# Performance work log

Hardware: AMD Instinct MI355X
Metric: run time of the kernel (lower is better)

The kernel has to match this reference:

```python
import jax, jax.numpy as jnp
import numpy as np
from jax import lax

T = 16384
L = 1024  # num_labels; START = L-2, STOP = L-1
NEG = -10000.0


def setup_inputs() -> dict:
    key = jax.random.key(0)
    k1, k2, k3 = jax.random.split(key, 3)
    pred_logits = jax.random.normal(k1, (T, L), dtype=jnp.float32)
    # gold tags avoid the reserved START (L-2) and STOP (L-1) tags
    ref = jax.random.randint(k2, (T,), 0, L - 2)
    transitions = jax.random.normal(k3, (L, L), dtype=jnp.float32)
    transitions = transitions.at[L - 2, :].set(NEG).at[L - 1, :].set(NEG)
    return {"pred_logits": pred_logits, "ref": ref, "transitions": transitions}


def reference(pred_logits, ref, transitions):
    num_labels = transitions.shape[0]
    START = num_labels - 2
    STOP = num_labels - 1

    # ---- forward algorithm (log-sum-exp recurrence over tags) ----
    init = jnp.full((num_labels,), NEG, dtype=pred_logits.dtype).at[START].set(0.0)

    def step(alpha, feat):
        # new_alpha[j] = logsumexp_i(alpha[i] + transitions[j, i]) + feat[j]
        new_alpha = jax.nn.logsumexp(alpha[None, :] + transitions, axis=1) + feat
        return new_alpha, None

    alpha, _ = lax.scan(step, init, pred_logits)
    forward_score = jax.nn.logsumexp(alpha + transitions[STOP])

    # ---- gold path score ----
    prev = jnp.concatenate([jnp.array([START], dtype=ref.dtype), ref[:-1]])
    trans_score = transitions[ref, prev].sum()
    emit_score = jnp.take_along_axis(pred_logits, ref[:, None], axis=1).sum()
    gold_score = trans_score + emit_score + transitions[STOP, ref[-1]]

    # torch returns shape (1,)
    return (forward_score - gold_score).reshape(1)
```

## Files before the change

### kernel.cpp

```cpp
#include <hip/hip_runtime.h>


#define TT    16384
#define LLAB  1024
#define NEGV  -10000.0
#define BQ    32
#define NCH   512
#define KCH   32
#define NPTY  8
#define AGT   __HIP_MEMORY_SCOPE_AGENT

typedef unsigned long long u64;
typedef unsigned int u32;
typedef unsigned short u16;
typedef _Float16 f16;
typedef _Float16 h2 __attribute__((ext_vector_type(2)));
typedef _Float16 f16x8 __attribute__((ext_vector_type(8)));
typedef float f32x4 __attribute__((ext_vector_type(4)));

__device__ __forceinline__ void pub64(u64* p, u64 v) {
  __hip_atomic_store(p, v, __ATOMIC_RELAXED, AGT);
}
__device__ __forceinline__ uint4 ld16_sc(const u32* p) {
  uint4 r;
  asm volatile("global_load_dwordx4 %0, %1, off sc0 sc1"
               : "=v"(r) : "v"(p) : "memory");
  return r;
}
__device__ __forceinline__ u32 pack2(float a, float b) {
  h2 h = {(f16)a, (f16)b};
  return __builtin_bit_cast(u32, h);
}
__device__ __forceinline__ float f16lo(u32 b) {
  return (float)__builtin_bit_cast(f16, (u16)(b & 0xFFFFu));
}
__device__ __forceinline__ float f16hi(u32 b) {
  return (float)__builtin_bit_cast(f16, (u16)(b >> 16));
}
__device__ __forceinline__ int swz(int c, int w) { return w ^ ((c & 7) << 2); }

__device__ __forceinline__ float max8(uint4 v) {
  float m = fmaxf(fmaxf(f16lo(v.x), f16hi(v.x)), fmaxf(f16lo(v.y), f16hi(v.y)));
  m = fmaxf(m, fmaxf(f16lo(v.z), f16hi(v.z)));
  m = fmaxf(m, fmaxf(f16lo(v.w), f16hi(v.w)));
  return m;
}

__global__ __launch_bounds__(256, 1) void crf_chunks(
    const float* __restrict__ pred, const float* __restrict__ trans,
    const int* __restrict__ ref, u32* __restrict__ pay, u32* __restrict__ fl,
    float* __restrict__ ybuf, float* __restrict__ zbuf,
    double* __restrict__ tlog, float* __restrict__ gold) {
  const int tid = threadIdx.x;
  const int wv = tid >> 6, l = tid & 63;
  const int lm = l & 15, lg = l >> 4;
  const int b = blockIdx.x;
  const int g = b & 31;
  const int party = b >> 5;
  const bool isFwd = (g < 16);
  const int cbase = (g & 15) * KCH;
  const int c1 = cbase + lm, c2 = cbase + lm + 16;
  const int tb1 = c1 * BQ, tb2 = c2 * BQ;
  const int wb = 128 * party + 32 * wv;

  f16x8 afrag0[32], afrag1[32];
  if (isFwd) {
    const float4* rp0 = (const float4*)&trans[(size_t)(wb + lm) * LLAB];
    const float4* rp1 = (const float4*)&trans[(size_t)(wb + 16 + lm) * LLAB];
#pragma unroll
    for (int kt = 0; kt < 32; ++kt) {
      float4 a = rp0[8 * kt + 2 * lg], c = rp0[8 * kt + 2 * lg + 1];
      f16x8 f;
      f[0] = (f16)__expf(a.x); f[1] = (f16)__expf(a.y);
      f[2] = (f16)__expf(a.z); f[3] = (f16)__expf(a.w);
      f[4] = (f16)__expf(c.x); f[5] = (f16)__expf(c.y);
      f[6] = (f16)__expf(c.z); f[7] = (f16)__expf(c.w);
      afrag0[kt] = f;
      a = rp1[8 * kt + 2 * lg]; c = rp1[8 * kt + 2 * lg + 1];
      f[0] = (f16)__expf(a.x); f[1] = (f16)__expf(a.y);
      f[2] = (f16)__expf(a.z); f[3] = (f16)__expf(a.w);
      f[4] = (f16)__expf(c.x); f[5] = (f16)__expf(c.y);
      f[6] = (f16)__expf(c.z); f[7] = (f16)__expf(c.w);
      afrag1[kt] = f;
    }
  } else {
    const int c0 = wb + lm, cc1 = wb + 16 + lm;
#pragma unroll
    for (int kt = 0; kt < 32; ++kt) {
      f16x8 f0, f1;
#pragma unroll
      for (int j = 0; j < 8; ++j) {
        int k = 32 * kt + 8 * lg + j;
        f0[j] = (f16)__expf(trans[(size_t)k * LLAB + c0]);
        f1[j] = (f16)__expf(trans[(size_t)k * LLAB + cc1]);
      }
      afrag0[kt] = f0; afrag1[kt] = f1;
    }
  }

  __shared__ __attribute__((aligned(16))) u32 qs[KCH * 512];
  __shared__ float smax[KCH];

  u32* gpay = pay + (size_t)g * 32768;
  u32* gfl  = fl + g * 512;

  {
    const int gc = tid >> 3, tp = tid & 7;
    float mm;
    if (isFwd) {
      uint4 ones = {0x3C003C00u, 0x3C003C00u, 0x3C003C00u, 0x3C003C00u};
#pragma unroll
      for (int i = 0; i < 16; ++i)
        *(uint4*)&qs[gc * 512 + swz(gc, 64 * tp + 4 * i)] = ones;
      mm = 1.0f;
    } else {
      int trow = (cbase + gc) * BQ + BQ - 1;
      const float4* pp = (const float4*)&pred[(size_t)trow * LLAB + 128 * tp];
      mm = 0.f;
#pragma unroll
      for (int i = 0; i < 16; ++i) {
        float4 e0 = pp[2 * i], e1 = pp[2 * i + 1];
        float a0 = __expf(e0.x), a1 = __expf(e0.y);
        float a2 = __expf(e0.z), a3 = __expf(e0.w);
        float a4 = __expf(e1.x), a5 = __expf(e1.y);
        float a6 = __expf(e1.z), a7 = __expf(e1.w);
        uint4 w4 = {pack2(a0, a1), pack2(a2, a3), pack2(a4, a5), pack2(a6, a7)};
        *(uint4*)&qs[gc * 512 + swz(gc, 64 * tp + 4 * i)] = w4;
        mm = fmaxf(mm, fmaxf(fmaxf(a0, a1), fmaxf(a2, a3)));
        mm = fmaxf(mm, fmaxf(fmaxf(a4, a5), fmaxf(a6, a7)));
      }
#pragma unroll
      for (int off = 1; off <= 4; off <<= 1) mm = fmaxf(mm, __shfl_xor(mm, off));
    }
    if (tp == 0) smax[gc] = mm;
  }
  __syncthreads();

  float4 fe1a, fe1b, fe2a, fe2b;
  {
    int t1 = isFwd ? tb1 : (tb1 + BQ - 2);
    int t2 = isFwd ? tb2 : (tb2 + BQ - 2);
    fe1a = *(const float4*)&pred[(size_t)t1 * LLAB + wb + 4 * lg];
    fe1b = *(const float4*)&pred[(size_t)t1 * LLAB + wb + 16 + 4 * lg];
    fe2a = *(const float4*)&pred[(size_t)t2 * LLAB + wb + 4 * lg];
    fe2b = *(const float4*)&pred[(size_t)t2 * LLAB + wb + 16 + 4 * lg];
  }

  const float C0 = 13359.727f;
  double up = 1.0;

  for (int s = 0; s < BQ; ++s) {
    const bool lastS = (s == BQ - 1);
    const int ps = s & 1;
    const u32 want = (u32)(s + 1);
    if (tid < KCH) up *= (double)smax[tid];
    const float i1 = 1.0f / (C0 * smax[lm]);
    const float i2 = 1.0f / (C0 * smax[lm + 16]);

    f32x4 a00 = {0.f, 0.f, 0.f, 0.f}, a01 = {0.f, 0.f, 0.f, 0.f};
    f32x4 a10 = {0.f, 0.f, 0.f, 0.f}, a11 = {0.f, 0.f, 0.f, 0.f};
#pragma unroll
    for (int kt = 0; kt < 32; ++kt) {
      f16x8 b1 = __builtin_bit_cast(f16x8,
          *(const uint4*)&qs[lm * 512 + swz(lm, 16 * kt + 4 * lg)]);
      f16x8 b2 = __builtin_bit_cast(f16x8,
          *(const uint4*)&qs[(lm + 16) * 512 + swz(lm + 16, 16 * kt + 4 * lg)]);
      a00 = __builtin_amdgcn_mfma_f32_16x16x32_f16(afrag0[kt], b1, a00, 0, 0, 0);
      a01 = __builtin_amdgcn_mfma_f32_16x16x32_f16(afrag1[kt], b1, a01, 0, 0, 0);
      a10 = __builtin_amdgcn_mfma_f32_16x16x32_f16(afrag0[kt], b2, a10, 0, 0, 0);
      a11 = __builtin_amdgcn_mfma_f32_16x16x32_f16(afrag1[kt], b2, a11, 0, 0, 0);
    }

    float4 n1a = fe1a, n1b = fe1b, n2a = fe2a, n2b = fe2b;
    if (!lastS) {
      int sn = s + 1;
      int t1 = isFwd ? (tb1 + sn) : (tb1 + BQ - 2 - sn);
      int t2 = isFwd ? (tb2 + sn) : (tb2 + BQ - 2 - sn);
      if (t1 < tb1) t1 = tb1;
      if (t2 < tb2) t2 = tb2;
      n1a = *(const float4*)&pred[(size_t)t1 * LLAB + wb + 4 * lg];
      n1b = *(const float4*)&pred[(size_t)t1 * LLAB + wb + 16 + 4 * lg];
      n2a = *(const float4*)&pred[(size_t)t2 * LLAB + wb + 4 * lg];
      n2b = *(const float4*)&pred[(size_t)t2 * LLAB + wb + 16 + 4 * lg];
    }

    const bool fold = isFwd || !lastS;
    float o00[4], o01[4], o10[4], o11[4];
    if (fold) {
      o00[0] = a00[0] * __expf(fe1a.x) * i1; o00[1] = a00[1] * __expf(fe1a.y) * i1;
      o00[2] = a00[2] * __expf(fe1a.z) * i1; o00[3] = a00[3] * __expf(fe1a.w) * i1;
      o01[0] = a01[0] * __expf(fe1b.x) * i1; o01[1] = a01[1] * __expf(fe1b.y) * i1;
      o01[2] = a01[2] * __expf(fe1b.z) * i1; o01[3] = a01[3] * __expf(fe1b.w) * i1;
      o10[0] = a10[0] * __expf(fe2a.x) * i2; o10[1] = a10[1] * __expf(fe2a.y) * i2;
      o10[2] = a10[2] * __expf(fe2a.z) * i2; o10[3] = a10[3] * __expf(fe2a.w) * i2;
      o11[0] = a11[0] * __expf(fe2b.x) * i2; o11[1] = a11[1] * __expf(fe2b.y) * i2;
      o11[2] = a11[2] * __expf(fe2b.z) * i2; o11[3] = a11[3] * __expf(fe2b.w) * i2;
    } else {
#pragma unroll
      for (int r = 0; r < 4; ++r) {
        o00[r] = a00[r] * i1; o01[r] = a01[r] * i1;
        o10[r] = a10[r] * i2; o11[r] = a11[r] * i2;
      }
    }

    if (lastS) {
      float* dst = isFwd ? ybuf : zbuf;
      size_t bb1 = (size_t)c1 * LLAB + wb + 4 * lg;
      size_t bb2 = (size_t)c2 * LLAB + wb + 4 * lg;
#pragma unroll
      for (int r = 0; r < 4; ++r) {
        dst[bb1 + r] = o00[r]; dst[bb1 + 16 + r] = o01[r];
        dst[bb2 + r] = o10[r]; dst[bb2 + 16 + r] = o11[r];
      }
      break;
    }

    const u32 q00 = pack2(o00[0], o00[1]), q01 = pack2(o00[2], o00[3]);
    const u32 q02 = pack2(o01[0], o01[1]), q03 = pack2(o01[2], o01[3]);
    const u32 q10 = pack2(o10[0], o10[1]), q11 = pack2(o10[2], o10[3]);
    const u32 q12 = pack2(o11[0], o11[1]), q13 = pack2(o11[2], o11[3]);
    {
      u64* op = (u64*)(gpay + (size_t)ps * 16384 + party * 2048);
      int i64 = lm * 32 + 8 * wv + lg;
      pub64(op + i64,       ((u64)q01 << 32) | q00);
      pub64(op + i64 + 4,   ((u64)q03 << 32) | q02);
      pub64(op + i64 + 512, ((u64)q11 << 32) | q10);
      pub64(op + i64 + 516, ((u64)q13 << 32) | q12);
    }
    __syncthreads();
    if (tid == 0)
      __hip_atomic_store(gfl + ps * 256 + party * 32, want, __ATOMIC_RELAXED, AGT);

    {
      int w = 16 * wv + 2 * lg;
      uint2 s0 = {q00, q01}, s1 = {q02, q03}, s2 = {q10, q11}, s3 = {q12, q13};
      *(uint2*)&qs[lm * 512 + swz(lm, party * 64 + w)] = s0;
      *(uint2*)&qs[lm * 512 + swz(lm, party * 64 + w + 8)] = s1;
      *(uint2*)&qs[(lm + 16) * 512 + swz(lm + 16, party * 64 + w)] = s2;
      *(uint2*)&qs[(lm + 16) * 512 + swz(lm + 16, party * 64 + w + 8)] = s3;
    }
    __syncthreads();

    {
      const u32* fp = gfl + ps * 256 + (l & 7) * 32;
      bool done = false;
      do {
        if (!done) done = (__hip_atomic_load(fp, __ATOMIC_RELAXED, AGT) >= want);
      } while (!__all(done));
    }

    {
      const u32* pb = gpay + (size_t)ps * 16384;
      const int c = tid >> 3, wbase = 8 * (tid & 7);
      uint4 gv[16];
#pragma unroll
      for (int p2 = 0; p2 < 8; ++p2) {
        if (p2 != party) {
          gv[2 * p2]     = ld16_sc(pb + p2 * 2048 + tid * 8);
          gv[2 * p2 + 1] = ld16_sc(pb + p2 * 2048 + tid * 8 + 4);
        }
      }
      asm volatile("s_waitcnt vmcnt(0)" ::: "memory");
      __builtin_amdgcn_sched_barrier(0);
      float mm = 0.f;
#pragma unroll
      for (int p2 = 0; p2 < 8; ++p2) {
        uint4 va, vb;
        if (p2 == party) {
          va = *(const uint4*)&qs[c * 512 + swz(c, p2 * 64 + wbase)];
          vb = *(const uint4*)&qs[c * 512 + swz(c, p2 * 64 + wbase + 4)];
        } else {
          va = gv[2 * p2]; vb = gv[2 * p2 + 1];
          *(uint4*)&qs[c * 512 + swz(c, p2 * 64 + wbase)] = va;
          *(uint4*)&qs[c * 512 + swz(c, p2 * 64 + wbase + 4)] = vb;
        }
        mm = fmaxf(mm, fmaxf(max8(va), max8(vb)));
      }
#pragma unroll
      for (int off = 1; off <= 4; off <<= 1) mm = fmaxf(mm, __shfl_xor(mm, off));
      if ((tid & 7) == 0) smax[c] = mm;
    }
    __syncthreads();
    fe1a = n1a; fe1b = n1b; fe2a = n2a; fe2b = n2b;
  }

  if (!isFwd && party == 0 && tid < KCH) tlog[cbase + tid] = log(up);

  if (tid < 64) {
    int t = b * 64 + tid;
    int r = ref[t];
    int prev = (t == 0) ? (LLAB - 2) : ref[t - 1];
    float v = trans[(size_t)r * LLAB + prev] + pred[(size_t)t * LLAB + r];
    if (t == TT - 1) v += trans[(size_t)(LLAB - 1) * LLAB + r];
#pragma unroll
    for (int off = 32; off >= 1; off >>= 1) v += __shfl_xor(v, off);
    if (tid == 0) atomicAdd(gold, v);
  }
}

__global__ __launch_bounds__(256) void crf_stitch(
    const float* __restrict__ ybuf, const float* __restrict__ zbuf,
    const double* __restrict__ tlog, const float* __restrict__ gold,
    double* __restrict__ dacc, u32* __restrict__ cnt, float* __restrict__ out) {
  const int tid = threadIdx.x;
  __shared__ double red[2][4];
  double local = 0.0;
  const double LC0 = log((double)13359.727f);
#pragma unroll
  for (int i = 0; i < 4; ++i) {
    const int cc = blockIdx.x * 4 + i;
    double na = 0.0, sa = 0.0;
    for (int j = tid; j < LLAB; j += 256) {
      double yv = (double)ybuf[(size_t)cc * LLAB + j];
      na += yv;
      double zz = (cc + 1 < NCH) ? (double)zbuf[(size_t)(cc + 1) * LLAB + j] : 1.0;
      sa += zz * yv;
    }
#pragma unroll
    for (int off = 32; off >= 1; off >>= 1) {
      na += __shfl_xor(na, off);
      sa += __shfl_xor(sa, off);
    }
    if ((tid & 63) == 0) { red[0][tid >> 6] = na; red[1][tid >> 6] = sa; }
    __syncthreads();
    if (tid == 0) {
      double n = red[0][0] + red[0][1] + red[0][2] + red[0][3];
      double sm = red[1][0] + red[1][1] + red[1][2] + red[1][3];
      local += log(sm) - log(n) + tlog[cc] + (double)BQ * LC0;
    }
    __syncthreads();
  }
  if (tid == 0) {
    atomicAdd(dacc, local);
    __threadfence();
    u32 old = atomicAdd(cnt, 1u);
    if (old == 127u) {
      __threadfence();
      double s = __hip_atomic_load(dacc, __ATOMIC_RELAXED, AGT);
      out[0] = (float)(s + log((double)zbuf[LLAB - 2]) + NEGV - (double)gold[0]);
    }
  }
}

extern "C" void kernel_launch(void* const* d_in, const int* in_sizes, int n_in,
                              void* d_out, int out_size, void* d_ws, size_t ws_size,
                              hipStream_t stream) {
  const float* pred  = (const float*)d_in[0];
  const int*   ref   = (const int*)d_in[1];
  const float* trans = (const float*)d_in[2];
  float* out = (float*)d_out;

  char* ws = (char*)d_ws;
  double* dacc = (double*)(ws + 0);
  float* gold  = (float*)(ws + 8);
  u32* cnt     = (u32*)(ws + 16);
  u32* fl      = (u32*)(ws + 256);
  u32* pay     = (u32*)(ws + 66560);
  size_t off = 66560 + (size_t)32 * 32768 * 4;
  float* ybuf = (float*)(ws + off); off += (size_t)NCH * LLAB * 4;
  float* zbuf = (float*)(ws + off); off += (size_t)NCH * LLAB * 4;
  double* tlog = (double*)(ws + off);

  hipMemsetAsync(ws, 0, 66560, stream);
  crf_chunks<<<256, 256, 0, stream>>>(pred, trans, ref, pay, fl, ybuf, zbuf,
                                      tlog, gold);
  crf_stitch<<<128, 256, 0, stream>>>(ybuf, zbuf, tlog, gold, dacc, cnt, out);
}
```

Baseline: 359.1 us.

## Use per-step exchange buffers with plain loads and single-wave sleeping flag poll

```diff
diff --git a/kernel.cpp b/kernel.cpp
--- a/kernel.cpp
+++ b/kernel.cpp
@@ -50,7 +50,7 @@
     const float* __restrict__ pred, const float* __restrict__ trans,
     const int* __restrict__ ref, u32* __restrict__ pay, u32* __restrict__ fl,
     float* __restrict__ ybuf, float* __restrict__ zbuf,
-    double* __restrict__ tlog, float* __restrict__ gold) {
+    double* __restrict__ tlog, float* __restrict__ gold, int fastp) {
   const int tid = threadIdx.x;
   const int wv = tid >> 6, l = tid & 63;
   const int lm = l & 15, lg = l >> 4;
@@ -101,8 +101,7 @@
   __shared__ __attribute__((aligned(16))) u32 qs[KCH * 512];
   __shared__ float smax[KCH];
 
-  u32* gpay = pay + (size_t)g * 32768;
-  u32* gfl  = fl + g * 512;
+  u32* gfl = fl + g * 16;
 
   {
     const int gc = tid >> 3, tp = tid & 7;
@@ -151,8 +150,11 @@
 
   for (int s = 0; s < BQ; ++s) {
     const bool lastS = (s == BQ - 1);
-    const int ps = s & 1;
     const u32 want = (u32)(s + 1);
+    const size_t stepBase = fastp
+        ? (size_t)16384 * ((size_t)g * (BQ - 1) + (size_t)s)
+        : (size_t)g * 32768 + (size_t)(s & 1) * 16384;
+    u32* sp = pay + stepBase;
     if (tid < KCH) up *= (double)smax[tid];
     const float i1 = 1.0f / (C0 * smax[lm]);
     const float i2 = 1.0f / (C0 * smax[lm + 16]);
@@ -220,7 +222,7 @@
     const u32 q10 = pack2(o10[0], o10[1]), q11 = pack2(o10[2], o10[3]);
     const u32 q12 = pack2(o11[0], o11[1]), q13 = pack2(o11[2], o11[3]);
     {
-      u64* op = (u64*)(gpay + (size_t)ps * 16384 + party * 2048);
+      u64* op = (u64*)sp + (size_t)party * 1024;
       int i64 = lm * 32 + 8 * wv + lg;
       pub64(op + i64,       ((u64)q01 << 32) | q00);
       pub64(op + i64 + 4,   ((u64)q03 << 32) | q02);
@@ -229,7 +231,7 @@
     }
     __syncthreads();
     if (tid == 0)
-      __hip_atomic_store(gfl + ps * 256 + party * 32, want, __ATOMIC_RELAXED, AGT);
+      __hip_atomic_store(gfl + party, want, __ATOMIC_RELAXED, AGT);
 
     {
       int w = 16 * wv + 2 * lg;
@@ -239,29 +241,41 @@
       *(uint2*)&qs[(lm + 16) * 512 + swz(lm + 16, party * 64 + w)] = s2;
       *(uint2*)&qs[(lm + 16) * 512 + swz(lm + 16, party * 64 + w + 8)] = s3;
     }
+
+    if (wv == 0) {
+      const u32* fp = gfl + (l & 7);
+      bool done = false;
+      while (true) {
+        if (!done) done = (__hip_atomic_load(fp, __ATOMIC_RELAXED, AGT) >= want);
+        if (__all(done)) break;
+        __builtin_amdgcn_s_sleep(2);
+      }
+    }
     __syncthreads();
 
     {
-      const u32* fp = gfl + ps * 256 + (l & 7) * 32;
-      bool done = false;
-      do {
-        if (!done) done = (__hip_atomic_load(fp, __ATOMIC_RELAXED, AGT) >= want);
-      } while (!__all(done));
-    }
-
-    {
-      const u32* pb = gpay + (size_t)ps * 16384;
+      const u32* pb = sp;
       const int c = tid >> 3, wbase = 8 * (tid & 7);
       uint4 gv[16];
-#pragma unroll
-      for (int p2 = 0; p2 < 8; ++p2) {
-        if (p2 != party) {
-          gv[2 * p2]     = ld16_sc(pb + p2 * 2048 + tid * 8);
-          gv[2 * p2 + 1] = ld16_sc(pb + p2 * 2048 + tid * 8 + 4);
+      if (fastp) {
+#pragma unroll
+        for (int p2 = 0; p2 < 8; ++p2) {
+          if (p2 != party) {
+            gv[2 * p2]     = *(const uint4*)(pb + p2 * 2048 + tid * 8);
+            gv[2 * p2 + 1] = *(const uint4*)(pb + p2 * 2048 + tid * 8 + 4);
+          }
         }
-      }
-      asm volatile("s_waitcnt vmcnt(0)" ::: "memory");
-      __builtin_amdgcn_sched_barrier(0);
+      } else {
+#pragma unroll
+        for (int p2 = 0; p2 < 8; ++p2) {
+          if (p2 != party) {
+            gv[2 * p2]     = ld16_sc(pb + p2 * 2048 + tid * 8);
+            gv[2 * p2 + 1] = ld16_sc(pb + p2 * 2048 + tid * 8 + 4);
+          }
+        }
+        asm volatile("s_waitcnt vmcnt(0)" ::: "memory");
+        __builtin_amdgcn_sched_barrier(0);
+      }
       float mm = 0.f;
 #pragma unroll
       for (int p2 = 0; p2 < 8; ++p2) {
@@ -355,14 +369,21 @@
   float* gold  = (float*)(ws + 8);
   u32* cnt     = (u32*)(ws + 16);
   u32* fl      = (u32*)(ws + 256);
-  u32* pay     = (u32*)(ws + 66560);
-  size_t off = 66560 + (size_t)32 * 32768 * 4;
+
+  const size_t payFast  = (size_t)32 * (BQ - 1) * 16384 * 4;
+  const size_t paySmall = (size_t)32 * 2 * 16384 * 4;
+  const size_t tail = (size_t)NCH * LLAB * 4 * 2 + 8192;
+  const int fastp = (ws_size >= 4096 + payFast + tail) ? 1 : 0;
+  const size_t paySz = fastp ? payFast : paySmall;
+
+  u32* pay = (u32*)(ws + 4096);
+  size_t off = 4096 + paySz;
   float* ybuf = (float*)(ws + off); off += (size_t)NCH * LLAB * 4;
   float* zbuf = (float*)(ws + off); off += (size_t)NCH * LLAB * 4;
   double* tlog = (double*)(ws + off);
 
-  hipMemsetAsync(ws, 0, 66560, stream);
+  hipMemsetAsync(ws, 0, 4096, stream);
   crf_chunks<<<256, 256, 0, stream>>>(pred, trans, ref, pay, fl, ybuf, zbuf,
-                                      tlog, gold);
+                                      tlog, gold, fastp);
   crf_stitch<<<128, 256, 0, stream>>>(ybuf, zbuf, tlog, gold, dacc, cnt, out);
 }
```

Result: faster. 343.9 us (-4.2%).
